# Optimization experiments

Measured on AMD Instinct MI355X. Metric: run time of the kernel, lower is better.

## Reference

```python
import jax, jax.numpy as jnp
import numpy as np

UNITS = 512
M = 8
INPUT_DIM = 512
BATCH = 2048


def setup_inputs() -> dict:
    key = jax.random.key(0)
    ks = jax.random.split(key, 9)
    D, U = INPUT_DIM, UNITS
    fused_dim = D + U
    def glorot(k, shape):
        lim = np.sqrt(6.0 / (shape[0] + shape[1])).astype(np.float32)
        return jax.random.uniform(k, shape, jnp.float32, -lim, lim)
    return {
        "inputs": jax.random.normal(ks[0], (BATCH, D), jnp.float32),
        "elapsed": jax.random.uniform(ks[1], (BATCH, 1), jnp.float32),
        "state": jax.random.normal(ks[2], (BATCH, U * M), jnp.float32),
        "W_r": glorot(ks[3], (fused_dim, U * M)),
        "b_r": jnp.zeros((U * M,), jnp.float32),
        "W_d": glorot(ks[4], (fused_dim, U)),
        "b_d": jnp.zeros((U,), jnp.float32),
        "W_u": glorot(ks[5], (fused_dim, U * M)),
        "b_u": jnp.zeros((U * M,), jnp.float32),
    }


def reference(inputs, elapsed, state, W_r, b_r, W_d, b_d, W_u, b_u):
    B = inputs.shape[0]
    # tau_i = 10**(i/2)  =>  ln_tau_i = i * 0.5 * ln(10)
    ln_tau_table = 0.5 * jnp.log(jnp.float32(10.0)) * jnp.arange(M, dtype=jnp.float32)  # [M]
    tau_table = jnp.exp(ln_tau_table)  # [M]

    h_hat = state.reshape(B, UNITS, M)            # [B, U, M]
    h = h_hat.sum(axis=2)                          # [B, U]
    fused = jnp.concatenate([inputs, h], axis=-1)  # [B, D+U]

    # retrieval gate: softmax over M buckets of -(ln_tau_r - table)^2
    ln_tau_r = (fused @ W_r + b_r).reshape(B, UNITS, M)
    rki = jax.nn.softmax(-jnp.square(ln_tau_r - ln_tau_table), axis=2)
    q_input = jnp.sum(rki * h_hat, axis=2)         # [B, U]

    # detect (candidate) with tanh
    reset_value = jnp.concatenate([inputs, q_input], axis=1)
    qk = jnp.tanh(reset_value @ W_d + b_d)[:, :, None]  # [B, U, 1]

    # update gate
    ln_tau_s = (fused @ W_u + b_u).reshape(B, UNITS, M)
    ski = jax.nn.softmax(-jnp.square(ln_tau_s - ln_tau_table), axis=2)

    # exponential decay per bucket: elapsed [B,1] / tau [M] -> [B, M]
    exp_term = jnp.exp(-elapsed / tau_table)[:, None, :]  # [B, 1, M]
    h_hat_next = ((1.0 - ski) * h_hat + ski * qk) * exp_term  # [B, U, M]

    h_next = h_hat_next.sum(axis=2)                # [B, U]
    return h_next, h_hat_next.reshape(B, UNITS * M)
```

## Files before the change

kernel.cpp:

```cpp
#include <hip/hip_runtime.h>
#include <hip/hip_fp16.h>
#include <cmath>

#define B_SZ 2048
#define D_IN 512
#define U_N  512
#define FD   1024
#define NRU  4096
#define NRU2 8192

typedef _Float16 f16x8 __attribute__((ext_vector_type(8)));
typedef float    f32x4 __attribute__((ext_vector_type(4)));

typedef const __attribute__((address_space(1))) void glb_cv;
typedef __attribute__((address_space(3))) void lds_v;

#define TAB_INIT {0.0f, 1.15129254649702f, 2.30258509299405f, \
                  3.45387763949107f, 4.60517018598809f, 5.75646273248511f, \
                  6.90775527898214f, 8.05904782547916f}

__global__ __launch_bounds__(256) void prep_conv_kernel(
    const float* __restrict__ inputs, const float* __restrict__ state,
    const float* __restrict__ W_r, const float* __restrict__ W_u,
    const float* __restrict__ W_d,
    __half* __restrict__ fused, __half* __restrict__ reset,
    __half* __restrict__ WruT, __half* __restrict__ WdT)
{
    const int bx = blockIdx.x;
    const int t  = threadIdx.x;

    if (bx < 4352) {
        const float* W;
        __half* Wt;
        int N, n, k0;
        if (bx < 2048) {
            W = W_r; Wt = WruT; N = NRU;
            n  = (bx & 15) * 256 + t;
            k0 = (bx >> 4) * 8;
        } else if (bx < 4096) {
            const int b2 = bx - 2048;
            W = W_u; Wt = WruT + (size_t)NRU * FD; N = NRU;
            n  = (b2 & 15) * 256 + t;
            k0 = (b2 >> 4) * 8;
        } else {
            const int b2 = bx - 4096;
            W = W_d; Wt = WdT; N = U_N;
            n  = (b2 & 1) * 256 + t;
            k0 = (b2 >> 1) * 8;
        }
        float v[8];
#pragma unroll
        for (int s = 0; s < 8; s++)
            v[s] = W[(size_t)(k0 + s) * N + n];
        f16x8 h;
#pragma unroll
        for (int s = 0; s < 8; s++)
            h[s] = (_Float16)v[s];
        *(f16x8*)(Wt + (size_t)n * FD + k0) = h;
        return;
    }

    const int b = bx - 4352;

    const float2 iv = *(const float2*)(inputs + (size_t)b * D_IN + t * 2);
    __half2 hv;
    hv.x = __float2half(iv.x);
    hv.y = __float2half(iv.y);
    *(__half2*)(fused + (size_t)b * FD + t * 2) = hv;
    *(__half2*)(reset + (size_t)b * FD + t * 2) = hv;

    const float4* sp = (const float4*)(state + (size_t)b * NRU + t * 16);
    float4 x0 = sp[0], x1 = sp[1], x2 = sp[2], x3 = sp[3];
    float s0 = (x0.x + x0.y) + (x0.z + x0.w) + (x1.x + x1.y) + (x1.z + x1.w);
    float s1 = (x2.x + x2.y) + (x2.z + x2.w) + (x3.x + x3.y) + (x3.z + x3.w);
    __half2 h2;
    h2.x = __float2half(s0);
    h2.y = __float2half(s1);
    *(__half2*)(fused + (size_t)b * FD + D_IN + t * 2) = h2;
}

__global__ __launch_bounds__(512, 2) void gemm_big(
    const __half* __restrict__ A, const __half* __restrict__ Bt,
    const float* __restrict__ b_r, const float* __restrict__ b_u,
    const float* __restrict__ state, __half* __restrict__ resetw,
    __half* __restrict__ skibuf)
{
    __shared__ __align__(16) char smem[131072];
    __half* SAh = (__half*)smem;

    const int t    = threadIdx.x;
    const int m0   = blockIdx.y << 8;
    const int n0   = blockIdx.x << 8;
    const int lane = t & 63;
    const int w    = t >> 6;
    const int wm16 = ((w >> 2) & 1) << 4;
    const int wn16 = (w & 3) << 4;
    const int m16  = lane & 15;
    const int quad = lane >> 4;
    const int g0   = (quad ^ (m16 & 7)) << 3;
    const int g1   = ((quad + 4) ^ (m16 & 7)) << 3;
    const int t8   = t << 3;
    const int trow = t >> 3;
    const int gcol = ((t & 7) ^ (trow & 7)) << 3;

    const __half* gA = A  + (size_t)(m0 + trow) * FD + gcol;
    const __half* gB = Bt + (size_t)(n0 + trow) * FD + gcol;

    f32x4 acc[8][4];
#pragma unroll
    for (int a1 = 0; a1 < 8; a1++)
#pragma unroll
        for (int a2 = 0; a2 < 4; a2++)
            acc[a1][a2] = (f32x4){0.f, 0.f, 0.f, 0.f};

#define BARRIER() __builtin_amdgcn_s_barrier()
#define PRIO1 __builtin_amdgcn_s_setprio(1)
#define PRIO0 __builtin_amdgcn_s_setprio(0)
#define WAITV(n) do { asm volatile("s_waitcnt vmcnt(" #n ")" ::: "memory"); \
                      __builtin_amdgcn_sched_barrier(0); } while (0)
#define WAITL() do { asm volatile("s_waitcnt lgkmcnt(0)" ::: "memory"); \
                     __builtin_amdgcn_sched_barrier(0); } while (0)

#define STAGE_A(buf, h, tt) do { \
        const __half* _s = gA + (size_t)((h) * 128) * FD + (tt) * 64; \
        __half* _d = SAh + (buf) * 32768 + (h) * 8192 + t8; \
        __builtin_amdgcn_global_load_lds((glb_cv*)_s, (lds_v*)_d, 16, 0, 0); \
        __builtin_amdgcn_global_load_lds((glb_cv*)(_s + (size_t)64 * FD), \
                                         (lds_v*)(_d + 4096), 16, 0, 0); } while (0)
#define STAGE_B(buf, h, tt) do { \
        const __half* _s = gB + (size_t)((h) * 128) * FD + (tt) * 64; \
        __half* _d = SAh + (buf) * 32768 + 16384 + (h) * 8192 + t8; \
        __builtin_amdgcn_global_load_lds((glb_cv*)_s, (lds_v*)_d, 16, 0, 0); \
        __builtin_amdgcn_global_load_lds((glb_cv*)(_s + (size_t)64 * FD), \
                                         (lds_v*)(_d + 4096), 16, 0, 0); } while (0)

#define READ_A(c, mh) do { _Pragma("unroll") \
    for (int mi2 = 0; mi2 < 4; mi2++) { \
        const __half* _ap = SAh + (c) * 32768 + \
            ((((mh) * 4 + mi2) * 32 + wm16 + m16) << 6); \
        af[mi2][0] = *(const f16x8*)(_ap + g0); \
        af[mi2][1] = *(const f16x8*)(_ap + g1); } } while (0)
#define READ_B_ALL(c) do { _Pragma("unroll") \
    for (int ni2 = 0; ni2 < 4; ni2++) { \
        const __half* _bp = SAh + (c) * 32768 + 16384 + \
            ((ni2 * 64 + wn16 + m16) << 6); \
        bf[ni2][0] = *(const f16x8*)(_bp + g0); \
        bf[ni2][1] = *(const f16x8*)(_bp + g1); } } while (0)

#define MFMA_Q(MH) do { _Pragma("unroll") \
    for (int ks = 0; ks < 2; ks++) { _Pragma("unroll") \
        for (int mi2 = 0; mi2 < 4; mi2++) { _Pragma("unroll") \
            for (int ni2 = 0; ni2 < 4; ni2++) { \
                acc[(MH)*4+mi2][ni2] = __builtin_amdgcn_mfma_f32_16x16x32_f16( \
                    af[mi2][ks], bf[ni2][ks], acc[(MH)*4+mi2][ni2], 0, 0, 0); } } } } while (0)

    STAGE_B(0, 0, 0); STAGE_B(0, 1, 0);
    STAGE_A(0, 0, 0); STAGE_A(0, 1, 0);
    STAGE_B(1, 0, 1); STAGE_B(1, 1, 1);
    WAITV(4);
    BARRIER();

#pragma unroll 1
    for (int i = 0; i < 8; i++) {
        const int t1 = (2 * i + 1) & 15, t2 = (2 * i + 2) & 15, t3 = (2 * i + 3) & 15;
        f16x8 af[4][2], bf[4][2];
        READ_B_ALL(0); READ_A(0, 0);
        STAGE_A(1, 0, t1); STAGE_A(1, 1, t1);
        WAITL(); PRIO1; MFMA_Q(0); PRIO0; BARRIER();
        READ_A(0, 1);
        STAGE_B(0, 0, t2); STAGE_B(0, 1, t2);
        WAITL(); PRIO1; MFMA_Q(1); PRIO0; WAITV(4); BARRIER();
        READ_B_ALL(1); READ_A(1, 0);
        STAGE_A(0, 0, t2); STAGE_A(0, 1, t2);
        WAITL(); PRIO1; MFMA_Q(0); PRIO0; BARRIER();
        READ_A(1, 1);
        STAGE_B(1, 0, t3); STAGE_B(1, 1, t3);
        WAITL(); PRIO1; MFMA_Q(1); PRIO0; WAITV(4); BARRIER();
    }

    WAITV(0);
    __syncthreads();

#undef BARRIER
#undef PRIO1
#undef PRIO0
#undef WAITV
#undef WAITL
#undef STAGE_A
#undef STAGE_B
#undef READ_A
#undef READ_B_ALL
#undef MFMA_Q

    float*  ebuf = (float*)smem;
    __half* qbuf = (__half*)(smem + 256 * 68 * 4);
    const bool is_r = (n0 < NRU);
    const float* bp = is_r ? b_r : b_u;
    const int n0r = is_r ? n0 : n0 - NRU;
    const float TAB[8] = TAB_INIT;

    for (int ni = 0; ni < 4; ni++) {
        const float bv = bp[n0r + ni * 64 + wn16 + m16];
#pragma unroll
        for (int mi = 0; mi < 8; mi++)
#pragma unroll
            for (int r = 0; r < 4; r++)
                ebuf[(mi * 32 + wm16 + quad * 4 + r) * 68 + wn16 + m16] =
                    acc[mi][ni][r] + bv;
        __syncthreads();

#pragma unroll
        for (int p = 0; p < 4; p++) {
            const int item = p * 512 + t;
            const int row = item >> 3, g = item & 7;
            const int b = m0 + row;
            const float* rp = ebuf + row * 68 + g * 8;
            float v[8];
            *(float4*)&v[0] = *(const float4*)rp;
            *(float4*)&v[4] = *(const float4*)(rp + 4);

            float e[8], sum = 0.f;
#pragma unroll
            for (int i2 = 0; i2 < 8; i2++) {
                float d = v[i2] - TAB[i2];
                e[i2] = __expf(-d * d);
                sum += e[i2];
            }
            const int colr = n0r + ni * 64 + g * 8;
            if (is_r) {
                const float4 h0 = *(const float4*)(state + (size_t)b * NRU + colr);
                const float4 h1 = *(const float4*)(state + (size_t)b * NRU + colr + 4);
                const float hv[8] = {h0.x, h0.y, h0.z, h0.w, h1.x, h1.y, h1.z, h1.w};
                float qn = 0.f;
#pragma unroll
                for (int i2 = 0; i2 < 8; i2++) qn += e[i2] * hv[i2];
                qbuf[row * 8 + g] = __float2half(qn / sum);
            } else {
                const float inv = 1.0f / sum;
                __half2 o[4];
#pragma unroll
                for (int i2 = 0; i2 < 4; i2++) {
                    o[i2].x = __float2half(e[2 * i2] * inv);
                    o[i2].y = __float2half(e[2 * i2 + 1] * inv);
                }
                *(uint4*)(skibuf + (size_t)b * NRU + colr) = *(uint4*)o;
            }
        }
        __syncthreads();
        if (is_r) {
            const int row = t >> 1, lg = (t & 1) << 2;
            uint2 qv = *(uint2*)(qbuf + row * 8 + lg);
            *(uint2*)(resetw + (size_t)(m0 + row) * FD + D_IN + (n0r >> 3) + ni * 8 + lg) = qv;
        }
    }
}

template <int BM, int EPI>
__global__ __launch_bounds__(256) void gemm_k(
    const __half* __restrict__ A, const __half* __restrict__ Bt,
    const float* __restrict__ biasA, const float* __restrict__ biasB, int nsplit,
    float* __restrict__ C, int Ncols,
    const float* __restrict__ state, __half* __restrict__ resetw,
    __half* __restrict__ skibuf, int K)
{
    extern __shared__ __align__(16) char smem[];
    __half* sA = (__half*)smem;
    __half* sB = (__half*)(smem + BM * 128);

    const int t    = threadIdx.x;
    const int m0   = blockIdx.y * BM;
    const int n0   = blockIdx.x << 7;
    const int lane = t & 63;
    const int w    = t >> 6;
    const int m16  = lane & 15;
    const int quad = lane >> 4;
    constexpr int MI = BM / 32;
    constexpr int IA = BM / 32;
    const int wm = (w & 1) * (BM / 2);
    const int wn = (w >> 1) << 6;

    f32x4 acc[MI][4];
#pragma unroll
    for (int i = 0; i < MI; i++)
#pragma unroll
        for (int j = 0; j < 4; j++)
#pragma unroll
            for (int r = 0; r < 4; r++) acc[i][j][r] = 0.f;

    const __half* gAp[IA];
    const __half* lAp[IA];
#pragma unroll
    for (int i = 0; i < IA; i++) {
        const int off = w * (BM * 32) + i * 1024 + lane * 16;
        const int row = off >> 7;
        const int g   = ((off & 127) >> 4) ^ (row & 7);
        gAp[i] = A + (size_t)(m0 + row) * K + g * 8;
        lAp[i] = sA + ((w * (BM * 32) + i * 1024) >> 1);
    }
    const __half* gBp[4];
    const __half* lBp[4];
#pragma unroll
    for (int i = 0; i < 4; i++) {
        const int off = w * 4096 + i * 1024 + lane * 16;
        const int row = off >> 7;
        const int g   = ((off & 127) >> 4) ^ (row & 7);
        gBp[i] = Bt + (size_t)(n0 + row) * K + g * 8;
        lBp[i] = sB + ((w * 4096 + i * 1024) >> 1);
    }

    for (int kt = 0; kt < K; kt += 64) {
        __syncthreads();
#pragma unroll
        for (int i = 0; i < IA; i++)
            __builtin_amdgcn_global_load_lds((glb_cv*)(gAp[i] + kt), (lds_v*)lAp[i], 16, 0, 0);
#pragma unroll
        for (int i = 0; i < 4; i++)
            __builtin_amdgcn_global_load_lds((glb_cv*)(gBp[i] + kt), (lds_v*)lBp[i], 16, 0, 0);
        __syncthreads();

#pragma unroll
        for (int s = 0; s < 2; s++) {
            f16x8 af[MI], bf[4];
#pragma unroll
            for (int mi = 0; mi < MI; mi++) {
                const int row = wm + mi * 16 + m16;
                const int gi  = (s * 4 + quad) ^ (row & 7);
                af[mi] = *(const f16x8*)(sA + row * 64 + gi * 8);
            }
#pragma unroll
            for (int ni = 0; ni < 4; ni++) {
                const int row = wn + ni * 16 + m16;
                const int gi  = (s * 4 + quad) ^ (row & 7);
                bf[ni] = *(const f16x8*)(sB + row * 64 + gi * 8);
            }
#pragma unroll
            for (int mi = 0; mi < MI; mi++)
#pragma unroll
                for (int ni = 0; ni < 4; ni++)
                    acc[mi][ni] = __builtin_amdgcn_mfma_f32_16x16x32_f16(
                        af[mi], bf[ni], acc[mi][ni], 0, 0, 0);
        }
    }

    if constexpr (EPI == 0) {
#pragma unroll
        for (int mi = 0; mi < MI; mi++) {
#pragma unroll
            for (int ni = 0; ni < 4; ni++) {
                const int col = n0 + wn + ni * 16 + m16;
                const float bv = biasA[col];
#pragma unroll
                for (int r = 0; r < 4; r++) {
                    const int row = m0 + wm + mi * 16 + quad * 4 + r;
                    C[(size_t)row * Ncols + col] = tanhf(acc[mi][ni][r] + bv);
                }
            }
        }
    }
}

__global__ __launch_bounds__(256) void final_kernel(
    const __half* __restrict__ skibuf, const float* __restrict__ state,
    const float* __restrict__ qk, const float* __restrict__ elapsed,
    float* __restrict__ out0, float* __restrict__ out1)
{
    const int idx = blockIdx.x * 256 + threadIdx.x;
    const int b = idx >> 9;
    const int u = idx & 511;

    const float INV_TAU[8] = {1.0f, 0.316227766016838f, 0.1f, 0.0316227766016838f,
                              0.01f, 0.00316227766016838f, 0.001f, 0.000316227766016838f};

    const uint4 sr = *(const uint4*)(skibuf + (size_t)b * NRU + u * 8);
    const __half2* sh = (const __half2*)&sr;
    float sk[8];
#pragma unroll
    for (int i = 0; i < 4; i++) {
        float2 f2 = __half22float2(sh[i]);
        sk[2 * i]     = f2.x;
        sk[2 * i + 1] = f2.y;
    }

    const float4* hh = (const float4*)(state + ((size_t)b * NRU + u * 8));
    float4 h0 = hh[0], h1 = hh[1];
    float h[8] = {h0.x, h0.y, h0.z, h0.w, h1.x, h1.y, h1.z, h1.w};

    const float q  = qk[(size_t)b * U_N + u];
    const float el = elapsed[b];

    float hn[8];
    float acc = 0.f;
#pragma unroll
    for (int i = 0; i < 8; i++) {
        const float et = __expf(-el * INV_TAU[i]);
        hn[i] = ((1.0f - sk[i]) * h[i] + sk[i] * q) * et;
        acc += hn[i];
    }

    float4* o = (float4*)(out1 + ((size_t)b * NRU + u * 8));
    o[0] = make_float4(hn[0], hn[1], hn[2], hn[3]);
    o[1] = make_float4(hn[4], hn[5], hn[6], hn[7]);
    out0[(size_t)b * U_N + u] = acc;
}

extern "C" void kernel_launch(void* const* d_in, const int* in_sizes, int n_in,
                              void* d_out, int out_size, void* d_ws, size_t ws_size,
                              hipStream_t stream)
{
    (void)in_sizes; (void)n_in; (void)out_size; (void)ws_size;

    const float* inputs  = (const float*)d_in[0];
    const float* elapsed = (const float*)d_in[1];
    const float* state   = (const float*)d_in[2];
    const float* W_r     = (const float*)d_in[3];
    const float* b_r     = (const float*)d_in[4];
    const float* W_d     = (const float*)d_in[5];
    const float* b_d     = (const float*)d_in[6];
    const float* W_u     = (const float*)d_in[7];
    const float* b_u     = (const float*)d_in[8];
    float* out = (float*)d_out;

    char* ws = (char*)d_ws;
    __half* fused  = (__half*)(ws);
    __half* reset  = (__half*)(ws + ((size_t)4  << 20));
    __half* WruT   = (__half*)(ws + ((size_t)8  << 20));
    __half* WdT    = (__half*)(ws + ((size_t)24 << 20));
    __half* skibuf = (__half*)(ws + ((size_t)25 << 20));
    float*  qk     = (float*) (ws + ((size_t)41 << 20));

    prep_conv_kernel<<<6400, 256, 0, stream>>>(inputs, state, W_r, W_u, W_d,
                                               fused, reset, WruT, WdT);

    gemm_big<<<dim3(NRU2 / 256, B_SZ / 256), 512, 0, stream>>>(
        fused, WruT, b_r, b_u, state, reset, skibuf);

    gemm_k<32, 0><<<dim3(U_N / 128, B_SZ / 32), 256, 20480, stream>>>(
        reset, WdT, b_d, nullptr, 1 << 30, qk, U_N, nullptr, nullptr, nullptr, FD);

    final_kernel<<<(B_SZ * U_N) / 256, 256, 0, stream>>>(skibuf, state, qk, elapsed, out,
                                                         out + (size_t)B_SZ * U_N);
}
```

Baseline: 198.5 us.

## Fuse final update into detect GEMM epilogue and tile weight transpose via LDS

The detect GEMM epilogue now applies tanh and then performs the full h_hat update and per-unit sum, writing both outputs directly. This removes the separate final kernel and the qk round trip through global memory. The weight transpose/convert in the prep kernel now stages 32x256 tiles in shared memory, so both the strided reads and the 16-byte writes are coalesced. The fused epilogue's per-thread loads of skibuf and state are strided by row and column and less coalesced than in the old elementwise kernel.

Measured after the change: 188.1 us (median of 2 runs). 5.3% less time.

```diff
diff --git a/kernel.cpp b/kernel.cpp
--- a/kernel.cpp
+++ b/kernel.cpp
@@ -18,6 +18,9 @@
 #define TAB_INIT {0.0f, 1.15129254649702f, 2.30258509299405f, \
                   3.45387763949107f, 4.60517018598809f, 5.75646273248511f, \
                   6.90775527898214f, 8.05904782547916f}
+
+#define INV_TAU_INIT {1.0f, 0.316227766016838f, 0.1f, 0.0316227766016838f, \
+                      0.01f, 0.00316227766016838f, 0.001f, 0.000316227766016838f}
 
 __global__ __launch_bounds__(256) void prep_conv_kernel(
     const float* __restrict__ inputs, const float* __restrict__ state,
@@ -29,38 +32,36 @@
     const int bx = blockIdx.x;
     const int t  = threadIdx.x;
 
-    if (bx < 4352) {
+    if (bx < 1088) {
+        __shared__ __half lt[32][264];
         const float* W;
         __half* Wt;
-        int N, n, k0;
-        if (bx < 2048) {
-            W = W_r; Wt = WruT; N = NRU;
-            n  = (bx & 15) * 256 + t;
-            k0 = (bx >> 4) * 8;
-        } else if (bx < 4096) {
-            const int b2 = bx - 2048;
-            W = W_u; Wt = WruT + (size_t)NRU * FD; N = NRU;
-            n  = (b2 & 15) * 256 + t;
-            k0 = (b2 >> 4) * 8;
-        } else {
-            const int b2 = bx - 4096;
-            W = W_d; Wt = WdT; N = U_N;
-            n  = (b2 & 1) * 256 + t;
-            k0 = (b2 >> 1) * 8;
-        }
-        float v[8];
-#pragma unroll
-        for (int s = 0; s < 8; s++)
-            v[s] = W[(size_t)(k0 + s) * N + n];
-        f16x8 h;
-#pragma unroll
-        for (int s = 0; s < 8; s++)
-            h[s] = (_Float16)v[s];
-        *(f16x8*)(Wt + (size_t)n * FD + k0) = h;
+        int N, b2;
+        if (bx < 512)       { W = W_r; Wt = WruT;                    N = NRU; b2 = bx; }
+        else if (bx < 1024) { W = W_u; Wt = WruT + (size_t)NRU * FD; N = NRU; b2 = bx - 512; }
+        else                { W = W_d; Wt = WdT;                     N = U_N; b2 = bx - 1024; }
+        const int n0 = (b2 >> 2) * 32;
+        const int kt = (b2 & 3) * 256;
+
+        const int n_off = t & 31, kg = t >> 5;
+#pragma unroll
+        for (int s = 0; s < 32; s++) {
+            const int kr = kg + s * 8;
+            lt[n_off][kr] = __float2half(W[(size_t)(kt + kr) * N + n0 + n_off]);
+        }
+        __syncthreads();
+
+        const int c = t & 31, ng = t >> 5;
+#pragma unroll
+        for (int p = 0; p < 4; p++) {
+            const int n = ng + p * 8;
+            f16x8 v = *(const f16x8*)&lt[n][c * 8];
+            *(f16x8*)(Wt + (size_t)(n0 + n) * FD + kt + c * 8) = v;
+        }
         return;
     }
 
-    const int b = bx - 4352;
+    const int b = bx - 1088;
 
     const float2 iv = *(const float2*)(inputs + (size_t)b * D_IN + t * 2);
     __half2 hv;
@@ -255,15 +256,16 @@
     }
 }
 
-template <int BM, int EPI>
-__global__ __launch_bounds__(256) void gemm_k(
+__global__ __launch_bounds__(256) void gemm_detect(
     const __half* __restrict__ A, const __half* __restrict__ Bt,
-    const float* __restrict__ biasA, const float* __restrict__ biasB, int nsplit,
-    float* __restrict__ C, int Ncols,
-    const float* __restrict__ state, __half* __restrict__ resetw,
-    __half* __restrict__ skibuf, int K)
+    const float* __restrict__ b_d,
+    const __half* __restrict__ skibuf, const float* __restrict__ state,
+    const float* __restrict__ elapsed,
+    float* __restrict__ out0, float* __restrict__ out1)
 {
-    extern __shared__ __align__(16) char smem[];
+    constexpr int BM = 32;
+    constexpr int K  = FD;
+    __shared__ __align__(16) char smem[20480];
     __half* sA = (__half*)smem;
     __half* sB = (__half*)(smem + BM * 128);
 
@@ -274,28 +276,23 @@
     const int w    = t >> 6;
     const int m16  = lane & 15;
     const int quad = lane >> 4;
-    constexpr int MI = BM / 32;
-    constexpr int IA = BM / 32;
     const int wm = (w & 1) * (BM / 2);
     const int wn = (w >> 1) << 6;
 
-    f32x4 acc[MI][4];
-#pragma unroll
-    for (int i = 0; i < MI; i++)
-#pragma unroll
-        for (int j = 0; j < 4; j++)
-#pragma unroll
-            for (int r = 0; r < 4; r++) acc[i][j][r] = 0.f;
-
-    const __half* gAp[IA];
-    const __half* lAp[IA];
-#pragma unroll
-    for (int i = 0; i < IA; i++) {
-        const int off = w * (BM * 32) + i * 1024 + lane * 16;
+    f32x4 acc[4];
+#pragma unroll
+    for (int j = 0; j < 4; j++)
+#pragma unroll
+        for (int r = 0; r < 4; r++) acc[j][r] = 0.f;
+
+    const __half* gAp;
+    const __half* lAp;
+    {
+        const int off = w * (BM * 32) + lane * 16;
         const int row = off >> 7;
         const int g   = ((off & 127) >> 4) ^ (row & 7);
-        gAp[i] = A + (size_t)(m0 + row) * K + g * 8;
-        lAp[i] = sA + ((w * (BM * 32) + i * 1024) >> 1);
+        gAp = A + (size_t)(m0 + row) * K + g * 8;
+        lAp = sA + ((w * (BM * 32)) >> 1);
     }
     const __half* gBp[4];
     const __half* lBp[4];
@@ -310,9 +307,7 @@
 
     for (int kt = 0; kt < K; kt += 64) {
         __syncthreads();
-#pragma unroll
-        for (int i = 0; i < IA; i++)
-            __builtin_amdgcn_global_load_lds((glb_cv*)(gAp[i] + kt), (lds_v*)lAp[i], 16, 0, 0);
+        __builtin_amdgcn_global_load_lds((glb_cv*)(gAp + kt), (lds_v*)lAp, 16, 0, 0);
 #pragma unroll
         for (int i = 0; i < 4; i++)
             __builtin_amdgcn_global_load_lds((glb_cv*)(gBp[i] + kt), (lds_v*)lBp[i], 16, 0, 0);
@@ -320,12 +315,11 @@
 
 #pragma unroll
         for (int s = 0; s < 2; s++) {
-            f16x8 af[MI], bf[4];
-#pragma unroll
-            for (int mi = 0; mi < MI; mi++) {
-                const int row = wm + mi * 16 + m16;
+            f16x8 af, bf[4];
+            {
+                const int row = wm + m16;
                 const int gi  = (s * 4 + quad) ^ (row & 7);
-                af[mi] = *(const f16x8*)(sA + row * 64 + gi * 8);
+                af = *(const f16x8*)(sA + row * 64 + gi * 8);
             }
 #pragma unroll
             for (int ni = 0; ni < 4; ni++) {
@@ -334,73 +328,55 @@
                 bf[ni] = *(const f16x8*)(sB + row * 64 + gi * 8);
             }
 #pragma unroll
-            for (int mi = 0; mi < MI; mi++)
-#pragma unroll
-                for (int ni = 0; ni < 4; ni++)
-                    acc[mi][ni] = __builtin_amdgcn_mfma_f32_16x16x32_f16(
-                        af[mi], bf[ni], acc[mi][ni], 0, 0, 0);
-        }
-    }
-
-    if constexpr (EPI == 0) {
-#pragma unroll
-        for (int mi = 0; mi < MI; mi++) {
-#pragma unroll
-            for (int ni = 0; ni < 4; ni++) {
-                const int col = n0 + wn + ni * 16 + m16;
-                const float bv = biasA[col];
-#pragma unroll
-                for (int r = 0; r < 4; r++) {
-                    const int row = m0 + wm + mi * 16 + quad * 4 + r;
-                    C[(size_t)row * Ncols + col] = tanhf(acc[mi][ni][r] + bv);
-                }
-            }
-        }
-    }
-}
-
-__global__ __launch_bounds__(256) void final_kernel(
-    const __half* __restrict__ skibuf, const float* __restrict__ state,
-    const float* __restrict__ qk, const float* __restrict__ elapsed,
-    float* __restrict__ out0, float* __restrict__ out1)
-{
-    const int idx = blockIdx.x * 256 + threadIdx.x;
-    const int b = idx >> 9;
-    const int u = idx & 511;
-
-    const float INV_TAU[8] = {1.0f, 0.316227766016838f, 0.1f, 0.0316227766016838f,
-                              0.01f, 0.00316227766016838f, 0.001f, 0.000316227766016838f};
-
-    const uint4 sr = *(const uint4*)(skibuf + (size_t)b * NRU + u * 8);
-    const __half2* sh = (const __half2*)&sr;
-    float sk[8];
-#pragma unroll
-    for (int i = 0; i < 4; i++) {
-        float2 f2 = __half22float2(sh[i]);
-        sk[2 * i]     = f2.x;
-        sk[2 * i + 1] = f2.y;
-    }
-
-    const float4* hh = (const float4*)(state + ((size_t)b * NRU + u * 8));
-    float4 h0 = hh[0], h1 = hh[1];
-    float h[8] = {h0.x, h0.y, h0.z, h0.w, h1.x, h1.y, h1.z, h1.w};
-
-    const float q  = qk[(size_t)b * U_N + u];
-    const float el = elapsed[b];
-
-    float hn[8];
-    float acc = 0.f;
-#pragma unroll
-    for (int i = 0; i < 8; i++) {
-        const float et = __expf(-el * INV_TAU[i]);
-        hn[i] = ((1.0f - sk[i]) * h[i] + sk[i] * q) * et;
-        acc += hn[i];
-    }
-
-    float4* o = (float4*)(out1 + ((size_t)b * NRU + u * 8));
-    o[0] = make_float4(hn[0], hn[1], hn[2], hn[3]);
-    o[1] = make_float4(hn[4], hn[5], hn[6], hn[7]);
-    out0[(size_t)b * U_N + u] = acc;
+            for (int ni = 0; ni < 4; ni++)
+                acc[ni] = __builtin_amdgcn_mfma_f32_16x16x32_f16(af, bf[ni], acc[ni], 0, 0, 0);
+        }
+    }
+
+    const float INV_TAU[8] = INV_TAU_INIT;
+    float bv[4];
+#pragma unroll
+    for (int ni = 0; ni < 4; ni++) bv[ni] = b_d[n0 + wn + ni * 16 + m16];
+
+#pragma unroll
+    for (int r = 0; r < 4; r++) {
+        const int row = m0 + wm + quad * 4 + r;
+        const float el = elapsed[row];
+        float et[8];
+#pragma unroll
+        for (int i = 0; i < 8; i++) et[i] = __expf(-el * INV_TAU[i]);
+
+#pragma unroll
+        for (int ni = 0; ni < 4; ni++) {
+            const int col = n0 + wn + ni * 16 + m16;
+            const float q = tanhf(acc[ni][r] + bv[ni]);
+
+            const uint4 sr = *(const uint4*)(skibuf + (size_t)row * NRU + col * 8);
+            const __half2* sh = (const __half2*)&sr;
+            float sk[8];
+#pragma unroll
+            for (int i = 0; i < 4; i++) {
+                float2 f2 = __half22float2(sh[i]);
+                sk[2 * i]     = f2.x;
+                sk[2 * i + 1] = f2.y;
+            }
+            const float4* hh = (const float4*)(state + ((size_t)row * NRU + col * 8));
+            float4 h0 = hh[0], h1 = hh[1];
+            float h[8] = {h0.x, h0.y, h0.z, h0.w, h1.x, h1.y, h1.z, h1.w};
+
+            float hn[8];
+            float accs = 0.f;
+#pragma unroll
+            for (int i = 0; i < 8; i++) {
+                hn[i] = ((1.0f - sk[i]) * h[i] + sk[i] * q) * et[i];
+                accs += hn[i];
+            }
+            float4* o = (float4*)(out1 + ((size_t)row * NRU + col * 8));
+            o[0] = make_float4(hn[0], hn[1], hn[2], hn[3]);
+            o[1] = make_float4(hn[4], hn[5], hn[6], hn[7]);
+            out0[(size_t)row * U_N + col] = accs;
+        }
+    }
 }
 
 extern "C" void kernel_launch(void* const* d_in, const int* in_sizes, int n_in,
@@ -426,17 +402,13 @@
     __half* WruT   = (__half*)(ws + ((size_t)8  << 20));
     __half* WdT    = (__half*)(ws + ((size_t)24 << 20));
     __half* skibuf = (__half*)(ws + ((size_t)25 << 20));
-    float*  qk     = (float*) (ws + ((size_t)41 << 20));
-
-    prep_conv_kernel<<<6400, 256, 0, stream>>>(inputs, state, W_r, W_u, W_d,
+
+    prep_conv_kernel<<<3136, 256, 0, stream>>>(inputs, state, W_r, W_u, W_d,
                                                fused, reset, WruT, WdT);
 
     gemm_big<<<dim3(NRU2 / 256, B_SZ / 256), 512, 0, stream>>>(
         fused, WruT, b_r, b_u, state, reset, skibuf);
 
-    gemm_k<32, 0><<<dim3(U_N / 128, B_SZ / 32), 256, 20480, stream>>>(
-        reset, WdT, b_d, nullptr, 1 << 30, qk, U_N, nullptr, nullptr, nullptr, FD);
-
-    final_kernel<<<(B_SZ * U_N) / 256, 256, 0, stream>>>(skibuf, state, qk, elapsed, out,
-                                                         out + (size_t)B_SZ * U_N);
+    gemm_detect<<<dim3(U_N / 128, B_SZ / 32), 256, 0, stream>>>(
+        reset, WdT, b_d, skibuf, state, elapsed, out, out + (size_t)B_SZ * U_N);
 }
```
